# Kernel optimization log

Hardware: AMD Instinct MI355X
Metric: run time of the kernel (lower is better)

## Reference

```python
import jax, jax.numpy as jnp
import numpy as np

NUM_HEADS = 16
ROPE_BASE = 10000.0


def _rope_cos_sin(seq_len, head_dim, dtype):
    inv_freq = 1.0 / (ROPE_BASE ** (jnp.arange(0, head_dim, 2, dtype=jnp.float32) / head_dim))
    t = jnp.arange(seq_len, dtype=jnp.float32)
    freqs = t[:, None] * inv_freq[None, :]          # [S, hd/2]
    emb = jnp.concatenate([freqs, freqs], axis=-1)  # [S, hd]
    return jnp.cos(emb).astype(dtype), jnp.sin(emb).astype(dtype)


def _rotate_half(x):
    x1, x2 = jnp.split(x, 2, axis=-1)
    return jnp.concatenate([-x2, x1], axis=-1)


def setup_inputs() -> dict:
    key = jax.random.key(0)
    k1, k2, k3 = jax.random.split(key, 3)
    B, S, D = 4, 2048, 1024
    x = jax.random.normal(k1, (B, S, D), dtype=jnp.float32)
    w_qkv = jax.random.normal(k2, (3 * D, D), dtype=jnp.float32) * (D ** -0.5)
    w_out = jax.random.normal(k3, (D, D), dtype=jnp.float32) * (D ** -0.5)
    return {"x": x, "w_qkv": w_qkv, "w_out": w_out}


def reference(x, w_qkv, w_out):
    B, S, D = x.shape
    H = NUM_HEADS
    hd = D // H
    scale = hd ** -0.5

    qkv = jnp.einsum('bsd,ed->bse', x, w_qkv)           # [B, S, 3D]
    qkv = qkv.reshape(B, S, 3, H, hd).transpose(2, 0, 3, 1, 4)  # [3, B, H, S, hd]
    q, k, v = qkv[0], qkv[1], qkv[2]

    cos, sin = _rope_cos_sin(S, hd, x.dtype)            # [S, hd] broadcast over B,H
    q = q * cos + _rotate_half(q) * sin
    k = k * cos + _rotate_half(k) * sin

    scores = jnp.einsum('bhqd,bhkd->bhqk', q, k) * scale  # [B, H, S, S]
    causal = jnp.tril(jnp.ones((S, S), dtype=bool))
    scores = jnp.where(causal, scores, jnp.finfo(scores.dtype).min)
    attn = jax.nn.softmax(scores, axis=-1)

    out = jnp.einsum('bhqk,bhkd->bhqd', attn, v)        # [B, H, S, hd]
    out = out.transpose(0, 2, 1, 3).reshape(B, S, D)
    out = jnp.einsum('bsd,ed->bse', out, w_out)
    return out
```

## Files before the change

### kernel.cpp

```cpp
#include <hip/hip_runtime.h>
#include <hip/hip_bf16.h>

typedef __bf16 bf16x8 __attribute__((ext_vector_type(8)));
typedef float f32x4 __attribute__((ext_vector_type(4)));
typedef __hip_bfloat16 bf16;

#define B_ 4
#define S_ 2048
#define D_ 1024
#define H_ 16
#define HD_ 64

__device__ __forceinline__ void gload16(const bf16* g, bf16* l) {
  __builtin_amdgcn_global_load_lds(
      (const __attribute__((address_space(1))) unsigned int*)g,
      (__attribute__((address_space(3))) unsigned int*)l, 16, 0, 0);
}

#define MFMA16(a, b, c) __builtin_amdgcn_mfma_f32_16x16x32_bf16((a), (b), (c), 0, 0, 0)

#define NX_ (B_ * S_ * D_)
#define NW1_ (3 * D_ * D_)
#define NW2_ (D_ * D_)
__global__ __launch_bounds__(256) void k_cvt3(const float* __restrict__ x,
                                              const float* __restrict__ w1,
                                              const float* __restrict__ w2,
                                              bf16* __restrict__ ox,
                                              bf16* __restrict__ o1,
                                              bf16* __restrict__ o2) {
  int i = (blockIdx.x * 256 + threadIdx.x) * 4;
  const float* in;
  bf16* out;
  if (i < NX_) {
    in = x; out = ox;
  } else if (i < NX_ + NW1_) {
    in = w1; out = o1; i -= NX_;
  } else {
    in = w2; out = o2; i -= NX_ + NW1_;
  }
  float4 v = *reinterpret_cast<const float4*>(in + i);
  alignas(8) bf16 t[4];
  t[0] = __float2bfloat16(v.x);
  t[1] = __float2bfloat16(v.y);
  t[2] = __float2bfloat16(v.z);
  t[3] = __float2bfloat16(v.w);
  *reinterpret_cast<uint2*>(out + i) = *reinterpret_cast<uint2*>(t);
}

__global__ __launch_bounds__(512) void k_qkv(const bf16* __restrict__ X,
                                             const bf16* __restrict__ W,
                                             bf16* __restrict__ Qw,
                                             bf16* __restrict__ Kw,
                                             bf16* __restrict__ Vtw) {
  __shared__ bf16 Al[2][128 * 64];
  __shared__ bf16 Bl[2][256 * 64];
  const int tid = threadIdx.x;
  const int wid = tid >> 6, lane = tid & 63, col = lane & 15, g = lane >> 4;
  const int wr = wid >> 2, wc = wid & 3;
  const int m0 = blockIdx.x * 128, n0 = blockIdx.y * 256;
  const int srow = tid >> 3;
  const int scol = (tid & 7) * 8;
  const int csrc = scol ^ ((srow & 7) * 8);
  const bf16* ga = X + (size_t)(m0 + srow) * 1024 + csrc;
  const bf16* gb = W + (size_t)(n0 + srow) * 1024 + csrc;
  const int ldst = srow * 64 + scol;
  const int rsw = (col & 7) * 8;
  f32x4 acc[4][4] = {};
#define QKV_STAGE_ALL(buf, k0)                               \
  do {                                                       \
    gload16(ga + (k0), &Al[buf][ldst]);                      \
    gload16(ga + (k0) + 64 * 1024, &Al[buf][ldst + 4096]);   \
    gload16(gb + (k0), &Bl[buf][ldst]);                      \
    gload16(gb + (k0) + 64 * 1024, &Bl[buf][ldst + 4096]);   \
    gload16(gb + (k0) + 128 * 1024, &Bl[buf][ldst + 8192]);  \
    gload16(gb + (k0) + 192 * 1024, &Bl[buf][ldst + 12288]); \
  } while (0)
  QKV_STAGE_ALL(0, 0);
  QKV_STAGE_ALL(1, 64);
  for (int kt = 0; kt < 16; ++kt) {
    const int c = kt & 1;
    if (kt < 15)
      asm volatile("s_waitcnt vmcnt(6)" ::: "memory");
    else
      asm volatile("s_waitcnt vmcnt(0)" ::: "memory");
    __builtin_amdgcn_s_barrier();
    const bf16* Ac = Al[c];
    const bf16* Bc = Bl[c];
    bf16x8 af[2][4], bfr[2][4];
#pragma unroll
    for (int kk = 0; kk < 2; ++kk) {
      const int ce = (kk * 32 + g * 8) ^ rsw;
#pragma unroll
      for (int m = 0; m < 4; ++m)
        af[kk][m] =
            *reinterpret_cast<const bf16x8*>(&Ac[(wr * 64 + m * 16 + col) * 64 + ce]);
#pragma unroll
      for (int n = 0; n < 4; ++n)
        bfr[kk][n] =
            *reinterpret_cast<const bf16x8*>(&Bc[(wc * 64 + n * 16 + col) * 64 + ce]);
    }
    __builtin_amdgcn_s_setprio(1);
#pragma unroll
    for (int m = 0; m < 4; ++m) {
      acc[m][0] = MFMA16(af[0][m], bfr[0][0], acc[m][0]);
      acc[m][1] = MFMA16(af[0][m], bfr[0][1], acc[m][1]);
    }
    __builtin_amdgcn_s_setprio(0);
    asm volatile("s_waitcnt lgkmcnt(0)" ::: "memory");
    __builtin_amdgcn_sched_barrier(0);
    __builtin_amdgcn_s_barrier();
    const bool more = (kt + 2 < 16);
    const int k2 = (kt + 2) * 64;
    if (more) {
      gload16(ga + k2, &Al[c][ldst]);
      gload16(ga + k2 + 64 * 1024, &Al[c][ldst + 4096]);
    }
    __builtin_amdgcn_s_setprio(1);
#pragma unroll
    for (int m = 0; m < 4; ++m) {
      acc[m][2] = MFMA16(af[0][m], bfr[0][2], acc[m][2]);
      acc[m][3] = MFMA16(af[0][m], bfr[0][3], acc[m][3]);
    }
    __builtin_amdgcn_s_setprio(0);
    if (more) {
      gload16(gb + k2, &Bl[c][ldst]);
      gload16(gb + k2 + 64 * 1024, &Bl[c][ldst + 4096]);
    }
    __builtin_amdgcn_s_setprio(1);
#pragma unroll
    for (int m = 0; m < 4; ++m) {
      acc[m][0] = MFMA16(af[1][m], bfr[1][0], acc[m][0]);
      acc[m][1] = MFMA16(af[1][m], bfr[1][1], acc[m][1]);
    }
    __builtin_amdgcn_s_setprio(0);
    if (more) {
      gload16(gb + k2 + 128 * 1024, &Bl[c][ldst + 8192]);
      gload16(gb + k2 + 192 * 1024, &Bl[c][ldst + 12288]);
    }
    __builtin_amdgcn_s_setprio(1);
#pragma unroll
    for (int m = 0; m < 4; ++m) {
      acc[m][2] = MFMA16(af[1][m], bfr[1][2], acc[m][2]);
      acc[m][3] = MFMA16(af[1][m], bfr[1][3], acc[m][3]);
    }
    __builtin_amdgcn_s_setprio(0);
  }
#undef QKV_STAGE_ALL
  const int e0 = n0 + wc * 64;
  const int which = e0 >> 10;
  const int h = (e0 >> 6) & 15;
  if (which == 2) {
#pragma unroll
    for (int m = 0; m < 4; ++m) {
      int mg = m0 + wr * 64 + m * 16 + g * 4;
      int b = mg >> 11, s = mg & 2047;
#pragma unroll
      for (int n = 0; n < 4; ++n) {
        int d = n * 16 + col;
        alignas(8) bf16 t[4];
#pragma unroll
        for (int r = 0; r < 4; ++r) t[r] = __float2bfloat16(acc[m][n][r]);
        *reinterpret_cast<uint2*>(&Vtw[((size_t)((b * 16 + h) * 64 + d) << 11) + s]) =
            *reinterpret_cast<uint2*>(t);
      }
    }
  } else {
    bf16* dst = which ? Kw : Qw;
    const float scale = which ? 1.0f : 0.18033688011112042f;
    const float fexp = -2.0f * 13.287712379549449f / 64.0f;
#pragma unroll
    for (int i = 0; i < 2; ++i) {
      int dlo = i * 16 + col;
      float invf = exp2f(fexp * (float)dlo);
#pragma unroll
      for (int m = 0; m < 4; ++m) {
        int mg = m0 + wr * 64 + m * 16 + g * 4;
        int b = mg >> 11;
        size_t rb = (size_t)(b * 16 + h) << 11;
#pragma unroll
        for (int r = 0; r < 4; ++r) {
          int s = (mg + r) & 2047;
          float sn, cs;
          __sincosf((float)s * invf, &sn, &cs);
          float lo = acc[m][i][r] * scale, hi = acc[m][i + 2][r] * scale;
          dst[((rb + s) << 6) + dlo] = __float2bfloat16(lo * cs - hi * sn);
          dst[((rb + s) << 6) + dlo + 32] = __float2bfloat16(hi * cs + lo * sn);
        }
      }
    }
  }
}

__global__ __launch_bounds__(512) void k_attn(const bf16* __restrict__ Q,
                                              const bf16* __restrict__ K,
                                              const bf16* __restrict__ Vt,
                                              bf16* __restrict__ AO) {
  __shared__ bf16 QPl[128][72];
  __shared__ bf16 Kl[64][72];
  __shared__ bf16 Vl[64][72];
  const int tid = threadIdx.x;
  const int wave = tid >> 6, lane = tid & 63, col = lane & 15, g = lane >> 4;
  const int bh = blockIdx.x;
  const size_t base = (size_t)bh << 17;
  const int r0 = tid >> 3, c0 = (tid & 7) * 8;
  const int b = bh >> 4, h = bh & 15;
  const int yy = blockIdx.y, a = yy >> 2, r_ = yy & 3;
  const int qt = (a == 0) ? (15 - r_) : (a == 1) ? (8 + (r_ ^ 2)) : (a == 2) ? (4 + (r_ ^ 1)) : r_;
  const int q0 = qt * 128;
  *reinterpret_cast<int4*>(&QPl[r0][c0]) =
      *reinterpret_cast<const int4*>(&Q[base + (size_t)(q0 + r0) * 64 + c0]);
  *reinterpret_cast<int4*>(&QPl[r0 + 64][c0]) =
      *reinterpret_cast<const int4*>(&Q[base + (size_t)(q0 + r0 + 64) * 64 + c0]);
  const int ktlim = 2 * qt + 1;
  const int ktmax = (q0 + wave * 16 + 15) >> 6;
  int4 kr = *reinterpret_cast<const int4*>(&K[base + (size_t)r0 * 64 + c0]);
  int4 vr = *reinterpret_cast<const int4*>(&Vt[base + (size_t)r0 * 2048 + c0]);
  *reinterpret_cast<int4*>(&Kl[r0][c0]) = kr;
  *reinterpret_cast<int4*>(&Vl[r0][c0]) = vr;
  kr = *reinterpret_cast<const int4*>(&K[base + (size_t)(64 + r0) * 64 + c0]);
  vr = *reinterpret_cast<const int4*>(&Vt[base + (size_t)r0 * 2048 + 64 + c0]);
  __syncthreads();
  bf16x8 qf[2];
#pragma unroll
  for (int kk = 0; kk < 2; ++kk)
    qf[kk] = *reinterpret_cast<const bf16x8*>(&QPl[wave * 16 + col][g * 8 + kk * 32]);
  float l_s = 0.0f;
  f32x4 o[4] = {};
  for (int kt = 0; kt <= ktlim; ++kt) {
    const int k0 = kt * 64;
    if (kt <= ktmax) {
      const int q = q0 + wave * 16 + col;
      const bool needmask = (k0 + 63 > q0 + wave * 16);
      __builtin_amdgcn_s_setprio(1);
#pragma unroll
      for (int n = 0; n < 4; ++n) {
        f32x4 s = {};
#pragma unroll
        for (int kk = 0; kk < 2; ++kk) {
          bf16x8 kf =
              *reinterpret_cast<const bf16x8*>(&Kl[n * 16 + col][g * 8 + kk * 32]);
          s = MFMA16(kf, qf[kk], s);
        }
        if (needmask) {
#pragma unroll
          for (int r = 0; r < 4; ++r)
            if (k0 + n * 16 + g * 4 + r > q) s[r] = -3e38f;
        }
        alignas(8) bf16 t[4];
#pragma unroll
        for (int r = 0; r < 4; ++r) {
          float p = exp2f(s[r]);
          l_s += p;
          t[r] = __float2bfloat16(p);
        }
        *reinterpret_cast<uint2*>(&QPl[wave * 16 + col][n * 16 + g * 4]) =
            *reinterpret_cast<uint2*>(t);
      }
#pragma unroll
      for (int kk = 0; kk < 2; ++kk) {
        bf16x8 pf =
            *reinterpret_cast<const bf16x8*>(&QPl[wave * 16 + col][g * 8 + kk * 32]);
#pragma unroll
        for (int n2 = 0; n2 < 4; ++n2) {
          bf16x8 vf =
              *reinterpret_cast<const bf16x8*>(&Vl[n2 * 16 + col][g * 8 + kk * 32]);
          o[n2] = MFMA16(pf, vf, o[n2]);
        }
      }
      __builtin_amdgcn_s_setprio(0);
    }
    __syncthreads();
    if (kt < ktlim) {
      *reinterpret_cast<int4*>(&Kl[r0][c0]) = kr;
      *reinterpret_cast<int4*>(&Vl[r0][c0]) = vr;
      if (kt + 2 <= ktlim) {
        const int k2 = k0 + 128;
        kr = *reinterpret_cast<const int4*>(&K[base + (size_t)(k2 + r0) * 64 + c0]);
        vr = *reinterpret_cast<const int4*>(&Vt[base + (size_t)r0 * 2048 + k2 + c0]);
      }
      __syncthreads();
    }
  }
  l_s += __shfl_xor(l_s, 16);
  l_s += __shfl_xor(l_s, 32);
#pragma unroll
  for (int r = 0; r < 4; ++r) {
    float inv = 1.0f / __shfl(l_s, (lane & 48) | (g * 4 + r));
    int s = q0 + wave * 16 + g * 4 + r;
#pragma unroll
    for (int n2 = 0; n2 < 4; ++n2)
      AO[((size_t)(b * 2048 + s) << 10) + h * 64 + n2 * 16 + col] =
          __float2bfloat16(o[n2][r] * inv);
  }
}

__global__ __launch_bounds__(512) void k_outproj(const bf16* __restrict__ A,
                                                 const bf16* __restrict__ W,
                                                 float* __restrict__ OUT) {
  __shared__ bf16 Al[2][128 * 64];
  __shared__ bf16 Bl[2][256 * 64];
  const int tid = threadIdx.x;
  const int wid = tid >> 6, lane = tid & 63, col = lane & 15, g = lane >> 4;
  const int wr = wid >> 2, wc = wid & 3;
  const int m0 = blockIdx.x * 128, n0 = blockIdx.y * 256;
  const int srow = tid >> 3;
  const int scol = (tid & 7) * 8;
  const int csrc = scol ^ ((srow & 7) * 8);
  const bf16* ga = A + (size_t)(m0 + srow) * 1024 + csrc;
  const bf16* gb = W + (size_t)(n0 + srow) * 1024 + csrc;
  const int ldst = srow * 64 + scol;
  const int rsw = (col & 7) * 8;
  f32x4 acc[4][4] = {};
#define OP_STAGE_ALL(buf, k0)                                \
  do {                                                       \
    gload16(ga + (k0), &Al[buf][ldst]);                      \
    gload16(ga + (k0) + 64 * 1024, &Al[buf][ldst + 4096]);   \
    gload16(gb + (k0), &Bl[buf][ldst]);                      \
    gload16(gb + (k0) + 64 * 1024, &Bl[buf][ldst + 4096]);   \
    gload16(gb + (k0) + 128 * 1024, &Bl[buf][ldst + 8192]);  \
    gload16(gb + (k0) + 192 * 1024, &Bl[buf][ldst + 12288]); \
  } while (0)
  OP_STAGE_ALL(0, 0);
  OP_STAGE_ALL(1, 64);
  for (int kt = 0; kt < 16; ++kt) {
    const int c = kt & 1;
    if (kt < 15)
      asm volatile("s_waitcnt vmcnt(6)" ::: "memory");
    else
      asm volatile("s_waitcnt vmcnt(0)" ::: "memory");
    __builtin_amdgcn_s_barrier();
    const bf16* Ac = Al[c];
    const bf16* Bc = Bl[c];
    bf16x8 af[2][4], bfr[2][4];
#pragma unroll
    for (int kk = 0; kk < 2; ++kk) {
      const int ce = (kk * 32 + g * 8) ^ rsw;
#pragma unroll
      for (int m = 0; m < 4; ++m)
        af[kk][m] =
            *reinterpret_cast<const bf16x8*>(&Ac[(wr * 64 + m * 16 + col) * 64 + ce]);
#pragma unroll
      for (int n = 0; n < 4; ++n)
        bfr[kk][n] =
            *reinterpret_cast<const bf16x8*>(&Bc[(wc * 64 + n * 16 + col) * 64 + ce]);
    }
    __builtin_amdgcn_s_setprio(1);
#pragma unroll
    for (int m = 0; m < 4; ++m) {
      acc[m][0] = MFMA16(af[0][m], bfr[0][0], acc[m][0]);
      acc[m][1] = MFMA16(af[0][m], bfr[0][1], acc[m][1]);
    }
    __builtin_amdgcn_s_setprio(0);
    asm volatile("s_waitcnt lgkmcnt(0)" ::: "memory");
    __builtin_amdgcn_sched_barrier(0);
    __builtin_amdgcn_s_barrier();
    const bool more = (kt + 2 < 16);
    const int k2 = (kt + 2) * 64;
    if (more) {
      gload16(ga + k2, &Al[c][ldst]);
      gload16(ga + k2 + 64 * 1024, &Al[c][ldst + 4096]);
    }
    __builtin_amdgcn_s_setprio(1);
#pragma unroll
    for (int m = 0; m < 4; ++m) {
      acc[m][2] = MFMA16(af[0][m], bfr[0][2], acc[m][2]);
      acc[m][3] = MFMA16(af[0][m], bfr[0][3], acc[m][3]);
    }
    __builtin_amdgcn_s_setprio(0);
    if (more) {
      gload16(gb + k2, &Bl[c][ldst]);
      gload16(gb + k2 + 64 * 1024, &Bl[c][ldst + 4096]);
    }
    __builtin_amdgcn_s_setprio(1);
#pragma unroll
    for (int m = 0; m < 4; ++m) {
      acc[m][0] = MFMA16(af[1][m], bfr[1][0], acc[m][0]);
      acc[m][1] = MFMA16(af[1][m], bfr[1][1], acc[m][1]);
    }
    __builtin_amdgcn_s_setprio(0);
    if (more) {
      gload16(gb + k2 + 128 * 1024, &Bl[c][ldst + 8192]);
      gload16(gb + k2 + 192 * 1024, &Bl[c][ldst + 12288]);
    }
    __builtin_amdgcn_s_setprio(1);
#pragma unroll
    for (int m = 0; m < 4; ++m) {
      acc[m][2] = MFMA16(af[1][m], bfr[1][2], acc[m][2]);
      acc[m][3] = MFMA16(af[1][m], bfr[1][3], acc[m][3]);
    }
    __builtin_amdgcn_s_setprio(0);
  }
#undef OP_STAGE_ALL
#pragma unroll
  for (int m = 0; m < 4; ++m)
#pragma unroll
    for (int n = 0; n < 4; ++n)
#pragma unroll
      for (int r = 0; r < 4; ++r)
        OUT[(size_t)(m0 + wr * 64 + m * 16 + g * 4 + r) * 1024 + n0 + wc * 64 + n * 16 +
            col] = acc[m][n][r];
}

extern "C" void kernel_launch(void* const* d_in, const int* in_sizes, int n_in,
                              void* d_out, int out_size, void* d_ws, size_t ws_size,
                              hipStream_t stream) {
  const float* x = (const float*)d_in[0];
  const float* wqkv = (const float*)d_in[1];
  const float* wout = (const float*)d_in[2];
  float* out = (float*)d_out;

  char* ws = (char*)d_ws;
  const size_t SZ_X = (size_t)B_ * S_ * D_ * 2;
  const size_t SZ_WQKV = (size_t)3 * D_ * D_ * 2;
  const size_t SZ_WOUT = (size_t)D_ * D_ * 2;
  const size_t SZ_T = (size_t)B_ * H_ * S_ * HD_ * 2;
  bf16* xb = (bf16*)(ws);
  bf16* wqkvb = (bf16*)(ws + SZ_X);
  bf16* woutb = (bf16*)(ws + SZ_X + SZ_WQKV);
  bf16* qws = (bf16*)(ws + SZ_X + SZ_WQKV + SZ_WOUT);
  bf16* kws = (bf16*)(ws + SZ_X + SZ_WQKV + SZ_WOUT + SZ_T);
  bf16* vtws = (bf16*)(ws + SZ_X + SZ_WQKV + SZ_WOUT + 2 * SZ_T);
  bf16* aob = (bf16*)(ws + SZ_X + SZ_WQKV + SZ_WOUT + 3 * SZ_T);

  const int NTOT4 = (NX_ + NW1_ + NW2_) / 4;
  k_cvt3<<<NTOT4 / 256, 256, 0, stream>>>(x, wqkv, wout, xb, wqkvb, woutb);

  k_qkv<<<dim3(64, 12), 512, 0, stream>>>(xb, wqkvb, qws, kws, vtws);
  k_attn<<<dim3(B_ * H_, 16), 512, 0, stream>>>(qws, kws, vtws, aob);
  k_outproj<<<dim3(64, 4), 512, 0, stream>>>(aob, woutb, out);
}
```

Measured before the change: 160.8 us.

## Load attention K/V/Q fragments directly from global memory, dropping LDS staging

The attention kernel stops staging K and V tiles through shared memory with register prefetch and double barriers. Each wave now reads its K and V MFMA fragments straight from global memory (relying on L1/L2 for reuse across the 8 waves), and Q fragments are loaded directly too. Only the P tile stays in LDS, and the per-iteration sync becomes a single raw s_barrier. This removes LDS traffic and sync overhead, at the cost of redundant global/cache reads across waves and no explicit prefetch to hide latency.

Result: slower. 355.1 us (+120.9%).

```diff
diff --git a/kernel.cpp b/kernel.cpp
--- a/kernel.cpp
+++ b/kernel.cpp
@@ -195,53 +195,42 @@
                                               const bf16* __restrict__ K,
                                               const bf16* __restrict__ Vt,
                                               bf16* __restrict__ AO) {
-  __shared__ bf16 QPl[128][72];
-  __shared__ bf16 Kl[64][72];
-  __shared__ bf16 Vl[64][72];
+  __shared__ bf16 Pl[128][72];
   const int tid = threadIdx.x;
   const int wave = tid >> 6, lane = tid & 63, col = lane & 15, g = lane >> 4;
   const int bh = blockIdx.x;
   const size_t base = (size_t)bh << 17;
-  const int r0 = tid >> 3, c0 = (tid & 7) * 8;
   const int b = bh >> 4, h = bh & 15;
   const int yy = blockIdx.y, a = yy >> 2, r_ = yy & 3;
   const int qt = (a == 0) ? (15 - r_) : (a == 1) ? (8 + (r_ ^ 2)) : (a == 2) ? (4 + (r_ ^ 1)) : r_;
   const int q0 = qt * 128;
-  *reinterpret_cast<int4*>(&QPl[r0][c0]) =
-      *reinterpret_cast<const int4*>(&Q[base + (size_t)(q0 + r0) * 64 + c0]);
-  *reinterpret_cast<int4*>(&QPl[r0 + 64][c0]) =
-      *reinterpret_cast<const int4*>(&Q[base + (size_t)(q0 + r0 + 64) * 64 + c0]);
+  const int qw = q0 + wave * 16;
+  const int q = qw + col;
+  const bf16* Qp = Q + base + (size_t)q * 64 + g * 8;
+  const bf16* Kp = K + base + (size_t)col * 64 + g * 8;
+  const bf16* Vp = Vt + base + (size_t)col * 2048 + g * 8;
+  bf16x8 qf[2];
+  qf[0] = *reinterpret_cast<const bf16x8*>(Qp);
+  qf[1] = *reinterpret_cast<const bf16x8*>(Qp + 32);
   const int ktlim = 2 * qt + 1;
-  const int ktmax = (q0 + wave * 16 + 15) >> 6;
-  int4 kr = *reinterpret_cast<const int4*>(&K[base + (size_t)r0 * 64 + c0]);
-  int4 vr = *reinterpret_cast<const int4*>(&Vt[base + (size_t)r0 * 2048 + c0]);
-  *reinterpret_cast<int4*>(&Kl[r0][c0]) = kr;
-  *reinterpret_cast<int4*>(&Vl[r0][c0]) = vr;
-  kr = *reinterpret_cast<const int4*>(&K[base + (size_t)(64 + r0) * 64 + c0]);
-  vr = *reinterpret_cast<const int4*>(&Vt[base + (size_t)r0 * 2048 + 64 + c0]);
-  __syncthreads();
-  bf16x8 qf[2];
-#pragma unroll
-  for (int kk = 0; kk < 2; ++kk)
-    qf[kk] = *reinterpret_cast<const bf16x8*>(&QPl[wave * 16 + col][g * 8 + kk * 32]);
+  const int ktmax = (qw + 15) >> 6;
   float l_s = 0.0f;
   f32x4 o[4] = {};
   for (int kt = 0; kt <= ktlim; ++kt) {
-    const int k0 = kt * 64;
     if (kt <= ktmax) {
-      const int q = q0 + wave * 16 + col;
-      const bool needmask = (k0 + 63 > q0 + wave * 16);
+      const int k0 = kt * 64;
+      const bool dmask = (kt == ktmax);
+      const bf16* Kt = Kp + (size_t)k0 * 64;
       __builtin_amdgcn_s_setprio(1);
 #pragma unroll
       for (int n = 0; n < 4; ++n) {
         f32x4 s = {};
 #pragma unroll
         for (int kk = 0; kk < 2; ++kk) {
-          bf16x8 kf =
-              *reinterpret_cast<const bf16x8*>(&Kl[n * 16 + col][g * 8 + kk * 32]);
+          bf16x8 kf = *reinterpret_cast<const bf16x8*>(Kt + n * 1024 + kk * 32);
           s = MFMA16(kf, qf[kk], s);
         }
-        if (needmask) {
+        if (dmask) {
 #pragma unroll
           for (int r = 0; r < 4; ++r)
             if (k0 + n * 16 + g * 4 + r > q) s[r] = -3e38f;
@@ -253,40 +242,30 @@
           l_s += p;
           t[r] = __float2bfloat16(p);
         }
-        *reinterpret_cast<uint2*>(&QPl[wave * 16 + col][n * 16 + g * 4]) =
+        *reinterpret_cast<uint2*>(&Pl[wave * 16 + col][n * 16 + g * 4]) =
             *reinterpret_cast<uint2*>(t);
       }
 #pragma unroll
       for (int kk = 0; kk < 2; ++kk) {
         bf16x8 pf =
-            *reinterpret_cast<const bf16x8*>(&QPl[wave * 16 + col][g * 8 + kk * 32]);
+            *reinterpret_cast<const bf16x8*>(&Pl[wave * 16 + col][g * 8 + kk * 32]);
 #pragma unroll
         for (int n2 = 0; n2 < 4; ++n2) {
           bf16x8 vf =
-              *reinterpret_cast<const bf16x8*>(&Vl[n2 * 16 + col][g * 8 + kk * 32]);
+              *reinterpret_cast<const bf16x8*>(Vp + n2 * 32768 + k0 + kk * 32);
           o[n2] = MFMA16(pf, vf, o[n2]);
         }
       }
       __builtin_amdgcn_s_setprio(0);
     }
-    __syncthreads();
-    if (kt < ktlim) {
-      *reinterpret_cast<int4*>(&Kl[r0][c0]) = kr;
-      *reinterpret_cast<int4*>(&Vl[r0][c0]) = vr;
-      if (kt + 2 <= ktlim) {
-        const int k2 = k0 + 128;
-        kr = *reinterpret_cast<const int4*>(&K[base + (size_t)(k2 + r0) * 64 + c0]);
-        vr = *reinterpret_cast<const int4*>(&Vt[base + (size_t)r0 * 2048 + k2 + c0]);
-      }
-      __syncthreads();
-    }
+    __builtin_amdgcn_s_barrier();
   }
   l_s += __shfl_xor(l_s, 16);
   l_s += __shfl_xor(l_s, 32);
 #pragma unroll
   for (int r = 0; r < 4; ++r) {
     float inv = 1.0f / __shfl(l_s, (lane & 48) | (g * 4 + r));
-    int s = q0 + wave * 16 + g * 4 + r;
+    int s = qw + g * 4 + r;
 #pragma unroll
     for (int n2 = 0; n2 < 4; ++n2)
       AO[((size_t)(b * 2048 + s) << 10) + h * 64 + n2 * 16 + col] =
```
